# Performance work log

Hardware: AMD Instinct MI355X
Metric: run time of the kernel (lower is better)

## Reference

```python
import jax, jax.numpy as jnp
import numpy as np

THRESHOLD = 0.9
EPS = 1e-12


def setup_inputs() -> dict:
    key = jax.random.key(0)
    ks = jax.random.split(key, 7)
    B, D_in, H1, H2, D_out = 8192, 256, 512, 256, 64
    # torch Linear default init ~ U(-1/sqrt(fan_in), 1/sqrt(fan_in)); randn scaled is fine as a stand-in
    def lin(k, out_f, in_f):
        return jax.random.normal(k, (out_f, in_f), dtype=jnp.float32) / np.sqrt(in_f)
    return {
        "x": jax.random.normal(ks[0], (B, D_in), dtype=jnp.float32),
        "W1": lin(ks[1], H1, D_in),
        "b1": jax.random.normal(ks[2], (H1,), dtype=jnp.float32) * 0.01,
        "W2": lin(ks[3], H2, H1),
        "b2": jax.random.normal(ks[4], (H2,), dtype=jnp.float32) * 0.01,
        "W3": lin(ks[5], D_out, H2),
        "b3": jax.random.normal(ks[6], (D_out,), dtype=jnp.float32) * 0.01,
    }


def reference(x, W1, b1, W2, b2, W3, b3):
    # MLP: Linear -> Tanh -> Linear -> Tanh -> Linear (no tanh on last)
    h1 = jnp.tanh(x @ W1.T + b1)          # [B, 512]
    h2 = jnp.tanh(h1 @ W2.T + b2)         # [B, 256]
    out = h2 @ W3.T + b3                  # [B, 64]

    # Pairwise state fidelity: (normalized dot)^2, thresholded adjacency (diag excluded)
    norms = jnp.linalg.norm(out, axis=-1, keepdims=True)  # [B, 1]
    normed = out / (norms + EPS)
    fid = (normed @ normed.T) ** 2                         # [B, B]
    adj = (fid >= THRESHOLD).astype(out.dtype)
    B = out.shape[0]
    adj = adj * (1.0 - jnp.eye(B, dtype=out.dtype))        # no self-edges (i < j pairs only)

    return adj @ out                                       # [B, 64]
```

## Files before the change

### kernel.cpp

```cpp
#include <hip/hip_runtime.h>
#include <hip/hip_bf16.h>
#include <math.h>

#define B_ROWS 8192
#define D_IN   256
#define H1_DIM 512
#define H2_DIM 256
#define D_OUT  64
#define EPSF   1e-12f
#define THRESH 0.9f

typedef __attribute__((ext_vector_type(8))) short short8;
typedef __attribute__((ext_vector_type(4))) float f32x4;

__device__ inline void pack8(const float* __restrict__ src, short* __restrict__ dh,
                             short* __restrict__ dm, int t, int C, int lgq) {
  const int lane = t & 63;
  const int g = t >> 6;
  const int q = g & ((1 << lgq) - 1);
  const int I = g >> lgq;
  const int row = I * 16 + (lane & 15);
  const int k0 = q * 32 + ((lane >> 4) << 3);
  const float* p = src + (size_t)row * C + k0;
  float4 a = *(const float4*)p;
  float4 b = *(const float4*)(p + 4);
  float v[8] = {a.x, a.y, a.z, a.w, b.x, b.y, b.z, b.w};
  short h8[8], m8[8];
#pragma unroll
  for (int e = 0; e < 8; ++e) {
    __hip_bfloat16 h = __float2bfloat16(v[e]);
    float hf = __bfloat162float(h);
    __hip_bfloat16 m = __float2bfloat16(v[e] - hf);
    h8[e] = *(short*)&h;
    m8[e] = *(short*)&m;
  }
  *(short8*)(dh + (size_t)t * 8) = *(short8*)h8;
  *(short8*)(dm + (size_t)t * 8) = *(short8*)m8;
}

__global__ __launch_bounds__(256)
void pack_inputs(const float* __restrict__ x, const float* __restrict__ W1,
                 const float* __restrict__ W2, const float* __restrict__ W3,
                 short* xh, short* xm, short* w1h, short* w1m,
                 short* w2h, short* w2m, short* w3h, short* w3m) {
  const int b = blockIdx.x;
  const int tid = threadIdx.x;
  if (b < 1024)       pack8(x,  xh,  xm,  b * 256 + tid, 256, 3);
  else if (b < 1088)  pack8(W1, w1h, w1m, (b - 1024) * 256 + tid, 256, 3);
  else if (b < 1152)  pack8(W2, w2h, w2m, (b - 1088) * 256 + tid, 512, 4);
  else                pack8(W3, w3h, w3m, (b - 1152) * 256 + tid, 256, 3);
}

template<int KSTEPS, int JT, int MODE>
__global__ __launch_bounds__(256, 2)
void mfma_gemm(const short* __restrict__ pAh, const short* __restrict__ pAm,
               const short* __restrict__ pBh, const short* __restrict__ pBm,
               const float* __restrict__ bias, float* __restrict__ Cout,
               short* __restrict__ dh, short* __restrict__ dm, int N,
               float* __restrict__ rz) {
  constexpr int ITB = 4;
  constexpr int BTJ = 2 * JT;
  constexpr int NITEMS = 2 * ITB + 2 * BTJ;
  constexpr int PER_WAVE = NITEMS / 4;
  constexpr int WCOL = 16 * JT + 4;
  union SM {
    struct {
      short Ah[2][ITB * 512];
      short Am[2][ITB * 512];
      short Bh[2][BTJ * 512];
      short Bm[2][BTJ * 512];
    } st;
    float wbuf[4 * 32 * WCOL];
  };
  __shared__ __align__(16) SM sm;
  __shared__ float nsum[2][64];
  __shared__ float invn[64];

  const int tid = threadIdx.x;
  const int wave = tid >> 6, lane = tid & 63;
  const int wi = wave >> 1, wj = wave & 1;
  const int bIt0 = blockIdx.x * ITB;
  const int bJt0 = blockIdx.y * BTJ;

  if constexpr (MODE == 2) {
    float4* rz4 = (float4*)(rz + (size_t)blockIdx.x * 64 * 64);
#pragma unroll
    for (int u = 0; u < 4; ++u)
      rz4[u * 256 + tid] = make_float4(0.f, 0.f, 0.f, 0.f);
  }

  f32x4 acc[2][JT];
#pragma unroll
  for (int a = 0; a < 2; ++a)
#pragma unroll
    for (int b = 0; b < JT; ++b) acc[a][b] = (f32x4){0.f, 0.f, 0.f, 0.f};

  auto stage = [&](int q, int bf) {
#pragma unroll
    for (int u = 0; u < PER_WAVE; ++u) {
      const int item = wave * PER_WAVE + u;
      const short* src;
      short* dst;
      if (item < 2 * ITB) {
        const int t = item >> 1;
        const int m = item & 1;
        src = (m ? pAm : pAh) + ((size_t)(bIt0 + t) * KSTEPS + q) * 512;
        dst = (m ? sm.st.Am : sm.st.Ah)[bf] + t * 512;
      } else {
        const int e = item - 2 * ITB;
        const int t = e >> 1;
        const int m = e & 1;
        src = (m ? pBm : pBh) + ((size_t)(bJt0 + t) * KSTEPS + q) * 512;
        dst = (m ? sm.st.Bm : sm.st.Bh)[bf] + t * 512;
      }
      __builtin_amdgcn_global_load_lds(
          (const __attribute__((address_space(1))) void*)(src + lane * 8),
          (__attribute__((address_space(3))) void*)dst, 16, 0, 0);
    }
  };

  stage(0, 0);
  for (int q = 0; q < KSTEPS; ++q) {
    __syncthreads();
    if (q + 1 < KSTEPS) stage(q + 1, (q + 1) & 1);
    const int bf = q & 1;
    short8 Ah[2], Am[2];
#pragma unroll
    for (int it = 0; it < 2; ++it) {
      Ah[it] = *(const short8*)(sm.st.Ah[bf] + (wi * 2 + it) * 512 + lane * 8);
      Am[it] = *(const short8*)(sm.st.Am[bf] + (wi * 2 + it) * 512 + lane * 8);
    }
    short8 Bh[JT], Bm[JT];
#pragma unroll
    for (int jt = 0; jt < JT; ++jt) {
      Bh[jt] = *(const short8*)(sm.st.Bh[bf] + (wj * JT + jt) * 512 + lane * 8);
      Bm[jt] = *(const short8*)(sm.st.Bm[bf] + (wj * JT + jt) * 512 + lane * 8);
    }
#pragma unroll
    for (int it = 0; it < 2; ++it)
#pragma unroll
      for (int jt = 0; jt < JT; ++jt) {
        acc[it][jt] = __builtin_amdgcn_mfma_f32_16x16x32_bf16(Ah[it], Bh[jt], acc[it][jt], 0, 0, 0);
        acc[it][jt] = __builtin_amdgcn_mfma_f32_16x16x32_bf16(Ah[it], Bm[jt], acc[it][jt], 0, 0, 0);
        acc[it][jt] = __builtin_amdgcn_mfma_f32_16x16x32_bf16(Am[it], Bh[jt], acc[it][jt], 0, 0, 0);
      }
  }
  __syncthreads();

  float bv[JT];
#pragma unroll
  for (int jt = 0; jt < JT; ++jt)
    bv[jt] = bias[(bJt0 + wj * JT + jt) * 16 + (lane & 15)];

  if constexpr (MODE == 1) {
#pragma unroll
    for (int it = 0; it < 2; ++it)
#pragma unroll
      for (int jt = 0; jt < JT; ++jt)
#pragma unroll
        for (int r = 0; r < 4; ++r) {
          const float val = tanhf(acc[it][jt][r] + bv[jt]);
          const int row_l = it * 16 + (lane >> 4) * 4 + r;
          const int col_l = jt * 16 + (lane & 15);
          sm.wbuf[(wave * 32 + row_l) * WCOL + col_l] = val;
        }
    __syncthreads();
  } else {
#pragma unroll
    for (int it = 0; it < 2; ++it)
#pragma unroll
      for (int r = 0; r < 4; ++r) {
        float sq = 0.f;
        const int row_l = it * 16 + (lane >> 4) * 4 + r;
#pragma unroll
        for (int jt = 0; jt < JT; ++jt) {
          const float val = acc[it][jt][r] + bv[jt];
          const int col_l = jt * 16 + (lane & 15);
          sm.wbuf[(wave * 32 + row_l) * WCOL + col_l] = val;
          const int row = (bIt0 + wi * 2 + it) * 16 + (lane >> 4) * 4 + r;
          Cout[(size_t)row * N + wj * (16 * JT) + col_l] = val;
          sq = fmaf(val, val, sq);
        }
#pragma unroll
        for (int m = 1; m < 16; m <<= 1) sq += __shfl_xor(sq, m, 64);
        if ((lane & 15) == 0) nsum[wj][wi * 32 + row_l] = sq;
      }
    __syncthreads();
    if (tid < 64) invn[tid] = 1.0f / (sqrtf(nsum[0][tid] + nsum[1][tid]) + EPSF);
    __syncthreads();
  }

  constexpr int QLMAX = (JT >= 2) ? (JT / 2) : 1;
#pragma unroll
  for (int itl = 0; itl < 2; ++itl)
#pragma unroll
    for (int ql = 0; ql < QLMAX; ++ql) {
      const int row_l = itl * 16 + (lane & 15);
      const int kl = ql * 32 + ((lane >> 4) << 3);
      const float* wp = &sm.wbuf[(wave * 32 + row_l) * WCOL + kl];
      const float scale = (MODE == 2) ? invn[wi * 32 + row_l] : 1.0f;
      float4 a = *(const float4*)wp;
      float4 b = *(const float4*)(wp + 4);
      float v[8] = {a.x, a.y, a.z, a.w, b.x, b.y, b.z, b.w};
      short h8[8], m8[8];
#pragma unroll
      for (int e = 0; e < 8; ++e) {
        const float sv = v[e] * scale;
        __hip_bfloat16 h = __float2bfloat16(sv);
        float hf = __bfloat162float(h);
        __hip_bfloat16 m = __float2bfloat16(sv - hf);
        h8[e] = *(short*)&h;
        m8[e] = *(short*)&m;
      }
      const int ItG = bIt0 + wi * 2 + itl;
      const int qG = (((bJt0 + wj * JT) * 16) + ql * 32) >> 5;
      const size_t off = ((size_t)(ItG * (N >> 5) + qG) * 64 + lane) * 8;
      *(short8*)(dh + off) = *(short8*)h8;
      *(short8*)(dm + off) = *(short8*)m8;
    }
}

#define JSPLIT 8
#define CT 8
#define NCHUNK (B_ROWS / JSPLIT / 16 / CT)

__global__ __launch_bounds__(256, 2)
void gram_accum(const short* __restrict__ vph, const short* __restrict__ vpm,
                const float* __restrict__ out, float* __restrict__ res) {
  __shared__ __align__(16) short lh[2][CT * 1024];
  __shared__ __align__(16) short lm[2][CT * 1024];
  const int tid = threadIdx.x;
  const int wave = tid >> 6;
  const int lane = tid & 63;
  const int i0 = blockIdx.x * 128;
  const int jbase = blockIdx.y * (B_ROWS / JSPLIT);

  short8 Ah[8][2], Am[8][2];
#pragma unroll
  for (int it = 0; it < 8; ++it) {
    const int It = (i0 >> 4) + it;
#pragma unroll
    for (int q = 0; q < 2; ++q) {
      Ah[it][q] = *(const short8*)(vph + (size_t)It * 1024 + q * 512 + lane * 8);
      Am[it][q] = *(const short8*)(vpm + (size_t)It * 1024 + q * 512 + lane * 8);
    }
  }

  auto stage = [&](int c, int bf) {
    const size_t base = ((size_t)(jbase >> 4) + c * CT) * 1024;
#pragma unroll
    for (int u = 0; u < 8; ++u) {
      const int item = wave * 8 + u;
      const short* src;
      short* dst;
      if (item < 16) { src = vph + base + item * 512; dst = lh[bf] + item * 512; }
      else           { src = vpm + base + (item - 16) * 512; dst = lm[bf] + (item - 16) * 512; }
      __builtin_amdgcn_global_load_lds(
          (const __attribute__((address_space(1))) void*)(src + lane * 8),
          (__attribute__((address_space(3))) void*)dst, 16, 0, 0);
    }
  };

  stage(0, 0);
  for (int c = 0; c < NCHUNK; ++c) {
    __syncthreads();
    if (c + 1 < NCHUNK) stage(c + 1, (c + 1) & 1);
    const int bf = c & 1;
#pragma unroll
    for (int t = 0; t < 2; ++t) {
      const int jt = wave * 2 + t;
      const int j0 = jbase + (c * CT + jt) * 16;
      short8 Bh0 = *(const short8*)(lh[bf] + jt * 1024 + lane * 8);
      short8 Bh1 = *(const short8*)(lh[bf] + jt * 1024 + 512 + lane * 8);
      short8 Bm0 = *(const short8*)(lm[bf] + jt * 1024 + lane * 8);
      short8 Bm1 = *(const short8*)(lm[bf] + jt * 1024 + 512 + lane * 8);
      f32x4 g[8];
#pragma unroll
      for (int it = 0; it < 8; ++it) g[it] = (f32x4){0.f, 0.f, 0.f, 0.f};
#pragma unroll
      for (int it = 0; it < 8; ++it) g[it] = __builtin_amdgcn_mfma_f32_16x16x32_bf16(Ah[it][0], Bh0, g[it], 0, 0, 0);
#pragma unroll
      for (int it = 0; it < 8; ++it) g[it] = __builtin_amdgcn_mfma_f32_16x16x32_bf16(Ah[it][1], Bh1, g[it], 0, 0, 0);
#pragma unroll
      for (int it = 0; it < 8; ++it) g[it] = __builtin_amdgcn_mfma_f32_16x16x32_bf16(Ah[it][0], Bm0, g[it], 0, 0, 0);
#pragma unroll
      for (int it = 0; it < 8; ++it) g[it] = __builtin_amdgcn_mfma_f32_16x16x32_bf16(Am[it][0], Bh0, g[it], 0, 0, 0);
#pragma unroll
      for (int it = 0; it < 8; ++it) g[it] = __builtin_amdgcn_mfma_f32_16x16x32_bf16(Ah[it][1], Bm1, g[it], 0, 0, 0);
#pragma unroll
      for (int it = 0; it < 8; ++it) g[it] = __builtin_amdgcn_mfma_f32_16x16x32_bf16(Am[it][1], Bh1, g[it], 0, 0, 0);
#pragma unroll
      for (int it = 0; it < 8; ++it) {
        const float m01 = fmaxf(g[it][0] * g[it][0], g[it][1] * g[it][1]);
        const float m23 = fmaxf(g[it][2] * g[it][2], g[it][3] * g[it][3]);
        if (fmaxf(m01, m23) >= THRESH) {
          const int j = j0 + (lane & 15);
          const float* __restrict__ oj = out + (size_t)j * D_OUT;
#pragma unroll
          for (int r = 0; r < 4; ++r) {
            if (g[it][r] * g[it][r] >= THRESH) {
              const int i = i0 + it * 16 + (lane >> 4) * 4 + r;
              if (i != j) {
                float* __restrict__ ri = res + (size_t)i * D_OUT;
                for (int k = 0; k < D_OUT; ++k) atomicAdd(&ri[k], oj[k]);
              }
            }
          }
        }
      }
    }
  }
}

#define MB (1024 * 1024)

extern "C" void kernel_launch(void* const* d_in, const int* in_sizes, int n_in,
                              void* d_out, int out_size, void* d_ws, size_t ws_size,
                              hipStream_t stream) {
  const float* x  = (const float*)d_in[0];
  const float* W1 = (const float*)d_in[1];
  const float* b1 = (const float*)d_in[2];
  const float* W2 = (const float*)d_in[3];
  const float* b2 = (const float*)d_in[4];
  const float* W3 = (const float*)d_in[5];
  const float* b3 = (const float*)d_in[6];
  float* res = (float*)d_out;

  char* ws = (char*)d_ws;
  short* xh  = (short*)(ws + 0 * MB);
  short* xm  = (short*)(ws + 4 * MB);
  short* h2h = (short*)(ws + 0 * MB);
  short* h2m = (short*)(ws + 4 * MB);
  short* h1h = (short*)(ws + 8 * MB);
  short* h1m = (short*)(ws + 16 * MB);
  float* out = (float*)(ws + 8 * MB);
  short* vph = (short*)(ws + 11 * MB);
  short* vpm = (short*)(ws + 12 * MB);
  short* w1h = (short*)(ws + 24 * MB);
  short* w1m = (short*)(ws + 24 * MB + 256 * 1024);
  short* w2h = (short*)(ws + 24 * MB + 512 * 1024);
  short* w2m = (short*)(ws + 24 * MB + 768 * 1024);
  short* w3h = (short*)(ws + 25 * MB);
  short* w3m = (short*)(ws + 25 * MB + 32 * 1024);

  pack_inputs<<<1160, 256, 0, stream>>>(x, W1, W2, W3, xh, xm, w1h, w1m, w2h, w2m, w3h, w3m);
  mfma_gemm<8, 4, 1><<<dim3(128, 4), 256, 0, stream>>>(
      xh, xm, w1h, w1m, b1, nullptr, h1h, h1m, H1_DIM, nullptr);
  mfma_gemm<16, 2, 1><<<dim3(128, 4), 256, 0, stream>>>(
      h1h, h1m, w2h, w2m, b2, nullptr, h2h, h2m, H2_DIM, nullptr);
  mfma_gemm<8, 2, 2><<<dim3(128, 1), 256, 0, stream>>>(
      h2h, h2m, w3h, w3m, b3, out, vph, vpm, D_OUT, res);
  gram_accum<<<dim3(B_ROWS / 128, JSPLIT), 256, 0, stream>>>(vph, vpm, out, res);
}
```

Baseline: 125.5 us.

## Use single-bf16 Gram screen with fp32 recheck of candidate pairs

```diff
diff --git a/kernel.cpp b/kernel.cpp
--- a/kernel.cpp
+++ b/kernel.cpp
@@ -9,6 +9,7 @@
 #define D_OUT  64
 #define EPSF   1e-12f
 #define THRESH 0.9f
+#define GUARD 0.94f
 
 typedef __attribute__((ext_vector_type(8))) short short8;
 typedef __attribute__((ext_vector_type(4))) float f32x4;
@@ -57,7 +58,7 @@
                const short* __restrict__ pBh, const short* __restrict__ pBm,
                const float* __restrict__ bias, float* __restrict__ Cout,
                short* __restrict__ dh, short* __restrict__ dm, int N,
-               float* __restrict__ rz) {
+               float* __restrict__ rz, float* __restrict__ invng) {
   constexpr int ITB = 4;
   constexpr int BTJ = 2 * JT;
   constexpr int NITEMS = 2 * ITB + 2 * BTJ;
@@ -186,7 +187,11 @@
         if ((lane & 15) == 0) nsum[wj][wi * 32 + row_l] = sq;
       }
     __syncthreads();
-    if (tid < 64) invn[tid] = 1.0f / (sqrtf(nsum[0][tid] + nsum[1][tid]) + EPSF);
+    if (tid < 64) {
+      const float iv = 1.0f / (sqrtf(nsum[0][tid] + nsum[1][tid]) + EPSF);
+      invn[tid] = iv;
+      invng[blockIdx.x * 64 + tid] = iv;
+    }
     __syncthreads();
   }
 
@@ -207,16 +212,18 @@
       for (int e = 0; e < 8; ++e) {
         const float sv = v[e] * scale;
         __hip_bfloat16 h = __float2bfloat16(sv);
-        float hf = __bfloat162float(h);
-        __hip_bfloat16 m = __float2bfloat16(sv - hf);
         h8[e] = *(short*)&h;
-        m8[e] = *(short*)&m;
+        if constexpr (MODE == 1) {
+          float hf = __bfloat162float(h);
+          __hip_bfloat16 m = __float2bfloat16(sv - hf);
+          m8[e] = *(short*)&m;
+        }
       }
       const int ItG = bIt0 + wi * 2 + itl;
       const int qG = (((bJt0 + wj * JT) * 16) + ql * 32) >> 5;
       const size_t off = ((size_t)(ItG * (N >> 5) + qG) * 64 + lane) * 8;
       *(short8*)(dh + off) = *(short8*)h8;
-      *(short8*)(dm + off) = *(short8*)m8;
+      if constexpr (MODE == 1) *(short8*)(dm + off) = *(short8*)m8;
     }
 }
 
@@ -225,36 +232,31 @@
 #define NCHUNK (B_ROWS / JSPLIT / 16 / CT)
 
 __global__ __launch_bounds__(256, 2)
-void gram_accum(const short* __restrict__ vph, const short* __restrict__ vpm,
-                const float* __restrict__ out, float* __restrict__ res) {
+void gram_accum(const short* __restrict__ vph, const float* __restrict__ out,
+                const float* __restrict__ invn, float* __restrict__ res) {
   __shared__ __align__(16) short lh[2][CT * 1024];
-  __shared__ __align__(16) short lm[2][CT * 1024];
   const int tid = threadIdx.x;
   const int wave = tid >> 6;
   const int lane = tid & 63;
   const int i0 = blockIdx.x * 128;
   const int jbase = blockIdx.y * (B_ROWS / JSPLIT);
 
-  short8 Ah[8][2], Am[8][2];
+  short8 Ah[8][2];
 #pragma unroll
   for (int it = 0; it < 8; ++it) {
     const int It = (i0 >> 4) + it;
 #pragma unroll
-    for (int q = 0; q < 2; ++q) {
+    for (int q = 0; q < 2; ++q)
       Ah[it][q] = *(const short8*)(vph + (size_t)It * 1024 + q * 512 + lane * 8);
-      Am[it][q] = *(const short8*)(vpm + (size_t)It * 1024 + q * 512 + lane * 8);
-    }
   }
 
   auto stage = [&](int c, int bf) {
     const size_t base = ((size_t)(jbase >> 4) + c * CT) * 1024;
 #pragma unroll
-    for (int u = 0; u < 8; ++u) {
-      const int item = wave * 8 + u;
-      const short* src;
-      short* dst;
-      if (item < 16) { src = vph + base + item * 512; dst = lh[bf] + item * 512; }
-      else           { src = vpm + base + (item - 16) * 512; dst = lm[bf] + (item - 16) * 512; }
+    for (int u = 0; u < 4; ++u) {
+      const int item = wave * 4 + u;
+      const short* src = vph + base + item * 512;
+      short* dst = lh[bf] + item * 512;
       __builtin_amdgcn_global_load_lds(
           (const __attribute__((address_space(1))) void*)(src + lane * 8),
           (__attribute__((address_space(3))) void*)dst, 16, 0, 0);
@@ -272,8 +274,6 @@
       const int j0 = jbase + (c * CT + jt) * 16;
       short8 Bh0 = *(const short8*)(lh[bf] + jt * 1024 + lane * 8);
       short8 Bh1 = *(const short8*)(lh[bf] + jt * 1024 + 512 + lane * 8);
-      short8 Bm0 = *(const short8*)(lm[bf] + jt * 1024 + lane * 8);
-      short8 Bm1 = *(const short8*)(lm[bf] + jt * 1024 + 512 + lane * 8);
       f32x4 g[8];
 #pragma unroll
       for (int it = 0; it < 8; ++it) g[it] = (f32x4){0.f, 0.f, 0.f, 0.f};
@@ -282,27 +282,31 @@
 #pragma unroll
       for (int it = 0; it < 8; ++it) g[it] = __builtin_amdgcn_mfma_f32_16x16x32_bf16(Ah[it][1], Bh1, g[it], 0, 0, 0);
 #pragma unroll
-      for (int it = 0; it < 8; ++it) g[it] = __builtin_amdgcn_mfma_f32_16x16x32_bf16(Ah[it][0], Bm0, g[it], 0, 0, 0);
-#pragma unroll
-      for (int it = 0; it < 8; ++it) g[it] = __builtin_amdgcn_mfma_f32_16x16x32_bf16(Am[it][0], Bh0, g[it], 0, 0, 0);
-#pragma unroll
-      for (int it = 0; it < 8; ++it) g[it] = __builtin_amdgcn_mfma_f32_16x16x32_bf16(Ah[it][1], Bm1, g[it], 0, 0, 0);
-#pragma unroll
-      for (int it = 0; it < 8; ++it) g[it] = __builtin_amdgcn_mfma_f32_16x16x32_bf16(Am[it][1], Bh1, g[it], 0, 0, 0);
-#pragma unroll
       for (int it = 0; it < 8; ++it) {
-        const float m01 = fmaxf(g[it][0] * g[it][0], g[it][1] * g[it][1]);
-        const float m23 = fmaxf(g[it][2] * g[it][2], g[it][3] * g[it][3]);
-        if (fmaxf(m01, m23) >= THRESH) {
+        const float m01 = fmaxf(fabsf(g[it][0]), fabsf(g[it][1]));
+        const float m23 = fmaxf(fabsf(g[it][2]), fabsf(g[it][3]));
+        if (fmaxf(m01, m23) >= GUARD) {
           const int j = j0 + (lane & 15);
+          const float ivj = invn[j];
           const float* __restrict__ oj = out + (size_t)j * D_OUT;
 #pragma unroll
           for (int r = 0; r < 4; ++r) {
-            if (g[it][r] * g[it][r] >= THRESH) {
+            if (fabsf(g[it][r]) >= GUARD) {
               const int i = i0 + it * 16 + (lane >> 4) * 4 + r;
               if (i != j) {
-                float* __restrict__ ri = res + (size_t)i * D_OUT;
-                for (int k = 0; k < D_OUT; ++k) atomicAdd(&ri[k], oj[k]);
+                const float* __restrict__ oi = out + (size_t)i * D_OUT;
+                float d = 0.f;
+                for (int k = 0; k < D_OUT; k += 4) {
+                  float4 a = *(const float4*)(oi + k);
+                  float4 b = *(const float4*)(oj + k);
+                  d = fmaf(a.x, b.x, d); d = fmaf(a.y, b.y, d);
+                  d = fmaf(a.z, b.z, d); d = fmaf(a.w, b.w, d);
+                }
+                const float nd = d * invn[i] * ivj;
+                if (nd * nd >= THRESH) {
+                  float* __restrict__ ri = res + (size_t)i * D_OUT;
+                  for (int k = 0; k < D_OUT; ++k) atomicAdd(&ri[k], oj[k]);
+                }
               }
             }
           }
@@ -333,9 +337,9 @@
   short* h2m = (short*)(ws + 4 * MB);
   short* h1h = (short*)(ws + 8 * MB);
   short* h1m = (short*)(ws + 16 * MB);
-  float* out = (float*)(ws + 8 * MB);
-  short* vph = (short*)(ws + 11 * MB);
-  short* vpm = (short*)(ws + 12 * MB);
+  float* out  = (float*)(ws + 8 * MB);
+  short* vph  = (short*)(ws + 11 * MB);
+  float* invn = (float*)(ws + 12 * MB);
   short* w1h = (short*)(ws + 24 * MB);
   short* w1m = (short*)(ws + 24 * MB + 256 * 1024);
   short* w2h = (short*)(ws + 24 * MB + 512 * 1024);
@@ -345,10 +349,10 @@
 
   pack_inputs<<<1160, 256, 0, stream>>>(x, W1, W2, W3, xh, xm, w1h, w1m, w2h, w2m, w3h, w3m);
   mfma_gemm<8, 4, 1><<<dim3(128, 4), 256, 0, stream>>>(
-      xh, xm, w1h, w1m, b1, nullptr, h1h, h1m, H1_DIM, nullptr);
+      xh, xm, w1h, w1m, b1, nullptr, h1h, h1m, H1_DIM, nullptr, nullptr);
   mfma_gemm<16, 2, 1><<<dim3(128, 4), 256, 0, stream>>>(
-      h1h, h1m, w2h, w2m, b2, nullptr, h2h, h2m, H2_DIM, nullptr);
+      h1h, h1m, w2h, w2m, b2, nullptr, h2h, h2m, H2_DIM, nullptr, nullptr);
   mfma_gemm<8, 2, 2><<<dim3(128, 1), 256, 0, stream>>>(
-      h2h, h2m, w3h, w3m, b3, out, vph, vpm, D_OUT, res);
-  gram_accum<<<dim3(B_ROWS / 128, JSPLIT), 256, 0, stream>>>(vph, vpm, out, res);
-}
+      h2h, h2m, w3h, w3m, b3, out, vph, nullptr, D_OUT, res, invn);
+  gram_accum<<<dim3(B_ROWS / 128, JSPLIT), 256, 0, stream>>>(vph, out, invn, res);
+}
```

Result: no change. 127.2 us (+1.3%).
